# Optimization experiments

Hardware: AMD Instinct MI355X
Metric: run time of the kernel (lower is better)

## Reference

```python
import jax, jax.numpy as jnp
from jax import lax
import numpy as np

FEAT_W = 52      # feature map width/height
IMG_W = 210      # input image width/height
SUB = IMG_W // FEAT_W  # = 4, sub_sample stride
N_ANCHOR = 9
NMS_THRESH = 0.7
PRE_NMS = 12000
POST_NMS = 2000
MIN_SIZE = 16.0


def make_anchors():
    # Faithful vectorization of generateAnchors: outer loop over ctr_x, inner over ctr_y,
    # then c unpacked as (ctr_y, ctr_x) = (x_val, y_val); ratios outer, scales inner.
    vals = (np.arange(SUB, (FEAT_W + 1) * SUB, SUB) - SUB // 2).astype(np.float64)  # 2,6,...,210
    cy = np.repeat(vals, FEAT_W)   # outer loop value -> anchor ctr_y
    cx = np.tile(vals, FEAT_W)     # inner loop value -> anchor ctr_x
    ratios = np.array([0.5, 1.0, 2.0])
    scales = np.array([4.0, 8.0, 16.0])
    h = (SUB * scales[None, :] * np.sqrt(ratios[:, None])).reshape(-1)      # (9,)
    w = (SUB * scales[None, :] * np.sqrt(1.0 / ratios[:, None])).reshape(-1)
    a = np.stack([cy[:, None] - h / 2.0, cx[:, None] - w / 2.0,
                  cy[:, None] + h / 2.0, cx[:, None] + w / 2.0], axis=-1)   # (2704, 9, 4)
    return a.reshape(-1, 4).astype(np.float32)  # (24336, 4) as [y1,x1,y2,x2]

_ANCHORS = jnp.asarray(make_anchors())


def _conv(x, w, b):
    y = lax.conv_general_dilated(x, w, (1, 1), 'SAME',
                                 dimension_numbers=('NCHW', 'OIHW', 'NCHW'))
    return y + b[None, :, None, None]


def propose_regions(locs, obj):
    # locs: (1, 24336, 4); obj: (1, 24336)
    anc = _ANCHORS
    ah = anc[:, 2] - anc[:, 0]
    aw = anc[:, 3] - anc[:, 1]
    acy = anc[:, 0] + 0.5 * ah
    acx = anc[:, 1] + 0.5 * aw
    l = locs[0]
    s = obj[0]
    cy = l[:, 0] * ah + acy
    cx = l[:, 1] * aw + acx
    hh = jnp.exp(l[:, 2]) * ah
    ww = jnp.exp(l[:, 3]) * aw
    roi = jnp.stack([cy - 0.5 * hh, cx - 0.5 * ww,
                     cy + 0.5 * hh, cx + 0.5 * ww], axis=1)
    roi = jnp.clip(roi, 0.0, float(IMG_W))
    hs = roi[:, 2] - roi[:, 0]
    ws = roi[:, 3] - roi[:, 1]
    valid = (hs >= MIN_SIZE) & (ws >= MIN_SIZE)
    # min_size filter folded into score masking; invalid boxes start suppressed
    masked = jnp.where(valid, s, -jnp.inf)
    order = jnp.argsort(-masked)[:PRE_NMS]
    boxes = roi[order]          # (PRE_NMS, 4) sorted by descending score
    v = valid[order]
    sgb = lax.stop_gradient(boxes)
    areas = (sgb[:, 3] - sgb[:, 1] + 1.0) * (sgb[:, 2] - sgb[:, 0] + 1.0)
    idxs = jnp.arange(PRE_NMS)

    def body(supp, i):
        b = sgb[i]
        yy1 = jnp.maximum(b[0], sgb[:, 0])
        xx1 = jnp.maximum(b[1], sgb[:, 1])
        yy2 = jnp.minimum(b[2], sgb[:, 2])
        xx2 = jnp.minimum(b[3], sgb[:, 3])
        inter = jnp.maximum(0.0, xx2 - xx1 + 1.0) * jnp.maximum(0.0, yy2 - yy1 + 1.0)
        iou = inter / (areas[i] + areas - inter)
        new = supp | ((iou > NMS_THRESH) & (idxs > i))
        return jnp.where(supp[i], supp, new), None

    supp, _ = lax.scan(body, ~v, idxs)  # greedy sequential NMS, fixed length
    keep = ~supp
    rank = jnp.cumsum(keep.astype(jnp.int32)) - 1
    write = keep & (rank < POST_NMS)
    tgt = jnp.where(write, rank, POST_NMS)  # overflow/dropped rows go to scrap slot
    out = jnp.zeros((POST_NMS + 1, 4), boxes.dtype).at[tgt].set(
        jnp.where(write[:, None], boxes, 0.0))
    return out[:POST_NMS]  # (2000, 4), zero-padded


def _forward(x, conv1_w, conv1_b, reg_w, reg_b, cls_w, cls_b):
    h = _conv(x, conv1_w, conv1_b)        # (1,256,52,52), no activation (as in source)
    reg = _conv(h, reg_w, reg_b)          # (1,36,52,52)
    cls = _conv(h, cls_w, cls_b)          # (1,18,52,52)
    locs = jnp.transpose(reg, (0, 2, 3, 1)).reshape(1, -1, 4)          # (1,24336,4)
    cls_t = jnp.transpose(cls, (0, 2, 3, 1))                            # (1,52,52,18)
    obj = cls_t.reshape(1, FEAT_W, FEAT_W, N_ANCHOR, 2)[..., 1].reshape(1, -1)
    cls_scores = cls_t.reshape(1, -1, 2)                                # (1,24336,2)
    rois = propose_regions(locs, obj)
    return rois, locs, cls_scores, obj


def setup_inputs() -> dict:
    key = jax.random.key(0)
    ks = jax.random.split(key, 4)
    x = jax.random.normal(ks[0], (1, 256, FEAT_W, FEAT_W), jnp.float32)
    conv1_w = 0.01 * jax.random.normal(ks[1], (256, 256, 3, 3), jnp.float32)
    conv1_b = jnp.zeros((256,), jnp.float32)
    reg_w = 0.01 * jax.random.normal(ks[2], (N_ANCHOR * 4, 256, 1, 1), jnp.float32)
    reg_b = jnp.zeros((N_ANCHOR * 4,), jnp.float32)
    cls_w = 0.01 * jax.random.normal(ks[3], (N_ANCHOR * 2, 256, 1, 1), jnp.float32)
    cls_b = jnp.zeros((N_ANCHOR * 2,), jnp.float32)
    return {"x": x, "conv1_w": conv1_w, "conv1_b": conv1_b,
            "reg_w": reg_w, "reg_b": reg_b, "cls_w": cls_w, "cls_b": cls_b}


def reference(x, conv1_w, conv1_b, reg_w, reg_b, cls_w, cls_b):
    rois, locs, cls_scores, obj = _forward(x, conv1_w, conv1_b, reg_w, reg_b, cls_w, cls_b)
    return (rois, locs, cls_scores, obj, cls_scores)
```

## Files before the change

### kernel.cpp

```cpp
#include <hip/hip_runtime.h>

typedef unsigned long long u64;
typedef unsigned int u32;

#define FEAT 52
#define NPIX 2704
#define NANC 24336
#define PRE  12000
#define POST 2000
#define ROWW 192
#define PADW 54
#define PADS 2916

#define ROIS_OFF 0
#define LOCS_OFF 8000
#define CLS_OFF  105344
#define OBJ_OFF  154016
#define CLS2_OFF 178352

#define OFF_W64   0ull
#define OFF_H64   4718592ull
#define OFF_REG64 10256384ull
#define OFF_SC64  11035136ull
#define OFF_ROI64 11229824ull
#define OFF_KEYS  12008576ull
#define OFF_SBOX  12270720ull
#define OFF_SAREA 12663936ull
#define OFF_SUPP  12762240ull
#define OFF_MASK  12763776ull
#define OFF_XPAD  OFF_MASK

__global__ __launch_bounds__(256) void k_prepx(const float* __restrict__ x,
                                               float* __restrict__ xpad) {
    int t = blockIdx.x * 256 + threadIdx.x;
    int ci = t / PADS, pos = t % PADS;
    int iy = pos / PADW, ix = pos % PADW;
    float v = 0.f;
    if (iy >= 1 && iy <= 52 && ix >= 1 && ix <= 52)
        v = x[ci * NPIX + (iy - 1) * FEAT + (ix - 1)];
    xpad[t] = v;
}

__global__ __launch_bounds__(256) void k_prepw(const float* __restrict__ w,
                                               double* __restrict__ w64) {
    int t = blockIdx.x * 256 + threadIdx.x;
    int j = t & 3;
    int r = t >> 2;
    int k = r % 9;
    int r2 = r / 9;
    int ci = r2 & 255;
    int g = r2 >> 8;
    w64[t] = (double)w[(((g * 4 + j) * 256) + ci) * 9 + k];
}

__global__ __launch_bounds__(256) void k_conv3(const float* __restrict__ xpad,
                                               const double* __restrict__ w64,
                                               const float* __restrict__ b,
                                               double* __restrict__ h64) {
    const int p = blockIdx.x * 256 + threadIdx.x;
    const int o0 = blockIdx.y * 4;
    if (p >= NPIX) return;
    const int y = p / FEAT, xq = p % FEAT;
    double a0 = (double)b[o0+0], a1 = (double)b[o0+1];
    double a2 = (double)b[o0+2], a3 = (double)b[o0+3];
    const float* xb = xpad + y * PADW + xq;
    const double* wb = w64 + (size_t)blockIdx.y * 9216;
    #pragma unroll 2
    for (int ci = 0; ci < 256; ++ci) {
        float f0 = xb[0],   f1 = xb[1],   f2 = xb[2];
        float f3 = xb[54],  f4 = xb[55],  f5 = xb[56];
        float f6 = xb[108], f7 = xb[109], f8 = xb[110];
        double xv[9];
        xv[0]=(double)f0; xv[1]=(double)f1; xv[2]=(double)f2;
        xv[3]=(double)f3; xv[4]=(double)f4; xv[5]=(double)f5;
        xv[6]=(double)f6; xv[7]=(double)f7; xv[8]=(double)f8;
        const double* wr = wb + ci * 36;
        #pragma unroll
        for (int k = 0; k < 9; ++k) {
            a0 += xv[k] * wr[4*k+0];
            a1 += xv[k] * wr[4*k+1];
            a2 += xv[k] * wr[4*k+2];
            a3 += xv[k] * wr[4*k+3];
        }
        xb += PADS;
    }
    h64[(o0+0)*NPIX + p] = a0;
    h64[(o0+1)*NPIX + p] = a1;
    h64[(o0+2)*NPIX + p] = a2;
    h64[(o0+3)*NPIX + p] = a3;
}

__global__ __launch_bounds__(64) void k_conv1(const double* __restrict__ h64,
                                              const float* __restrict__ regw,
                                              const float* __restrict__ regb,
                                              const float* __restrict__ clsw,
                                              const float* __restrict__ clsb,
                                              float* __restrict__ out,
                                              double* __restrict__ reg64,
                                              double* __restrict__ score64) {
    const int g = blockIdx.y;
    const int p = blockIdx.x * 64 + threadIdx.x;
    if (p >= NPIX) return;
    const bool isreg = (g < 4);
    const float* wbase = isreg ? (regw + g * 9 * 256) : (clsw + (g - 4) * 9 * 256);
    const float* bbase = isreg ? (regb + g * 9)       : (clsb + (g - 4) * 9);
    double acc[9];
    #pragma unroll
    for (int j = 0; j < 9; ++j) acc[j] = (double)bbase[j];
    #pragma unroll 4
    for (int ci = 0; ci < 256; ++ci) {
        double h = h64[ci * NPIX + p];
        #pragma unroll
        for (int j = 0; j < 9; ++j)
            acc[j] += h * (double)wbase[j * 256 + ci];
    }
    #pragma unroll
    for (int j = 0; j < 9; ++j) {
        int oc = g * 9 + j;
        float v = (float)acc[j];
        if (isreg) {
            out[LOCS_OFF + p*36 + oc] = v;
            reg64[p*36 + oc] = acc[j];
        } else {
            int c = oc - 36;
            out[CLS_OFF  + p*18 + c] = v;
            out[CLS2_OFF + p*18 + c] = v;
            if (c & 1) {
                out[OBJ_OFF + p*9 + (c >> 1)] = v;
                score64[p*9 + (c >> 1)] = acc[j];
            }
        }
    }
}

__global__ __launch_bounds__(256) void k_decode(const double* __restrict__ reg64,
                                                const double* __restrict__ score64,
                                                double* __restrict__ roi64,
                                                u64* __restrict__ keys) {
    int t = blockIdx.x * 256 + threadIdx.x;
    if (t >= NANC) { keys[t] = ~0ull; return; }
    int pos = t / 9, a = t % 9;
    int py = pos / FEAT, px = pos % FEAT;
    int ri = a / 3, si = a % 3;
    double rat = (ri == 0) ? 0.5 : (ri == 1 ? 1.0 : 2.0);
    double scl = (si == 0) ? 4.0 : (si == 1 ? 8.0 : 16.0);
    double hA = 4.0 * scl * sqrt(rat);
    double wA = 4.0 * scl * sqrt(1.0 / rat);
    double cy0 = 4.0 * py + 2.0, cx0 = 4.0 * px + 2.0;
    float y1f = (float)(cy0 - hA / 2.0), x1f = (float)(cx0 - wA / 2.0);
    float y2f = (float)(cy0 + hA / 2.0), x2f = (float)(cx0 + wA / 2.0);
    double ah = (double)y2f - (double)y1f, aw = (double)x2f - (double)x1f;
    double acy = (double)y1f + 0.5 * ah, acx = (double)x1f + 0.5 * aw;
    double l0 = reg64[4*t+0], l1 = reg64[4*t+1], l2 = reg64[4*t+2], l3 = reg64[4*t+3];
    double cy = l0 * ah + acy, cx = l1 * aw + acx;
    double hh = exp(l2) * ah,  ww = exp(l3) * aw;
    double r0 = fmin(fmax(cy - 0.5*hh, 0.0), 210.0);
    double r1 = fmin(fmax(cx - 0.5*ww, 0.0), 210.0);
    double r2 = fmin(fmax(cy + 0.5*hh, 0.0), 210.0);
    double r3 = fmin(fmax(cx + 0.5*ww, 0.0), 210.0);
    roi64[4*t+0] = r0; roi64[4*t+1] = r1; roi64[4*t+2] = r2; roi64[4*t+3] = r3;
    bool valid = (r2 - r0 >= 16.0) && (r3 - r1 >= 16.0);
    double m = valid ? score64[t] : -__builtin_huge_val();
    long long ll = __double_as_longlong(m);
    u64 u = (u64)ll;
    u64 mono = (ll < 0) ? ~u : (u ^ 0x8000000000000000ull);
    keys[t] = ((~mono) & 0xFFFFFFFFFFFF0000ull) | (u64)t;
}

__global__ __launch_bounds__(1024) void k_sortA(u64* __restrict__ keys) {
    __shared__ u64 s[8192];
    const int base = blockIdx.x * 8192;
    for (int t = threadIdx.x; t < 8192; t += 1024) s[t] = keys[base + t];
    __syncthreads();
    for (int k = 2; k <= 8192; k <<= 1) {
        for (int j = k >> 1; j > 0; j >>= 1) {
            for (int q = threadIdx.x; q < 4096; q += 1024) {
                int i = ((q & ~(j-1)) << 1) | (q & (j-1));
                int l = i | j;
                bool asc = (((base + i) & k) == 0);
                u64 A = s[i], B = s[l];
                bool sw = asc ? (A > B) : (A < B);
                if (sw) { s[i] = B; s[l] = A; }
            }
            __syncthreads();
        }
    }
    for (int t = threadIdx.x; t < 8192; t += 1024) keys[base + t] = s[t];
}

__global__ __launch_bounds__(1024) void k_sortB(u64* __restrict__ keys, int k) {
    __shared__ u64 s[8192];
    const int base = blockIdx.x * 8192;
    for (int t = threadIdx.x; t < 8192; t += 1024) s[t] = keys[base + t];
    __syncthreads();
    for (int j = 4096; j > 0; j >>= 1) {
        for (int q = threadIdx.x; q < 4096; q += 1024) {
            int i = ((q & ~(j-1)) << 1) | (q & (j-1));
            int l = i | j;
            bool asc = (((base + i) & k) == 0);
            u64 A = s[i], B = s[l];
            bool sw = asc ? (A > B) : (A < B);
            if (sw) { s[i] = B; s[l] = A; }
        }
        __syncthreads();
    }
    for (int t = threadIdx.x; t < 8192; t += 1024) keys[base + t] = s[t];
}

__global__ __launch_bounds__(256) void k_sortG(u64* __restrict__ keys, int k, int j) {
    int t = blockIdx.x * 256 + threadIdx.x;
    int i = ((t & ~(j-1)) << 1) | (t & (j-1));
    int l = i | j;
    bool asc = ((i & k) == 0);
    u64 A = keys[i], B = keys[l];
    bool sw = asc ? (A > B) : (A < B);
    if (sw) { keys[i] = B; keys[l] = A; }
}

__global__ __launch_bounds__(256) void k_gather(const u64* __restrict__ keys,
                                                const double* __restrict__ roi64,
                                                double* __restrict__ sbox,
                                                double* __restrict__ sarea,
                                                u64* __restrict__ suppinit) {
    int p = blockIdx.x * 256 + threadIdx.x;
    bool sup = true;
    if (p < PRE) {
        int idx = (int)(keys[p] & 0xFFFFull);
        double b0 = roi64[4*idx+0], b1 = roi64[4*idx+1];
        double b2 = roi64[4*idx+2], b3 = roi64[4*idx+3];
        sbox[4*p+0] = b0; sbox[4*p+1] = b1; sbox[4*p+2] = b2; sbox[4*p+3] = b3;
        sarea[p] = (b3 - b1 + 1.0) * (b2 - b0 + 1.0);
        sup = !((b2 - b0 >= 16.0) && (b3 - b1 >= 16.0));
    } else {
        sbox[4*p+0] = 0.0; sbox[4*p+1] = 0.0; sbox[4*p+2] = 0.0; sbox[4*p+3] = 0.0;
        sarea[p] = 1.0;
    }
    u64 ball = __ballot(sup);
    if ((threadIdx.x & 63) == 0) suppinit[p >> 6] = ball;
}

__global__ __launch_bounds__(256) void k_mask(const double* __restrict__ sbox,
                                              const double* __restrict__ sarea,
                                              u64* __restrict__ mask) {
    const int jt = blockIdx.x, it = blockIdx.y;
    const int ib = it * 64, jb0 = jt * 1024;
    if (jb0 + 1023 <= ib) {
        for (int t = threadIdx.x; t < 1024; t += 256) {
            int ti = t >> 4, w = t & 15;
            int i = ib + ti;
            if (i < PRE) mask[(size_t)i * ROWW + jt*16 + w] = 0ull;
        }
        return;
    }
    __shared__ double jbx[4096];
    __shared__ double jar[1024];
    for (int t = threadIdx.x; t < 4096; t += 256) jbx[t] = sbox[(size_t)jb0*4 + t];
    for (int t = threadIdx.x; t < 1024; t += 256) jar[t] = sarea[jb0 + t];
    __syncthreads();
    int ti = threadIdx.x >> 2;
    int i = ib + ti;
    if (i >= PRE) return;
    double iy1 = sbox[4*i+0], ix1 = sbox[4*i+1], iy2 = sbox[4*i+2], ix2 = sbox[4*i+3];
    double iar = sarea[i];
    for (int w = (threadIdx.x & 3); w < 16; w += 4) {
        u64 bits = 0ull;
        int q0 = w * 64;
        for (int l = 0; l < 64; ++l) {
            int q = q0 + l;
            double jy1 = jbx[4*q+0], jx1 = jbx[4*q+1], jy2 = jbx[4*q+2], jx2 = jbx[4*q+3];
            double yy1 = fmax(iy1, jy1), xx1 = fmax(ix1, jx1);
            double yy2 = fmin(iy2, jy2), xx2 = fmin(ix2, jx2);
            double iw = fmax(xx2 - xx1 + 1.0, 0.0);
            double ih = fmax(yy2 - yy1 + 1.0, 0.0);
            double inter = iw * ih;
            bool s = ((jb0 + q) > i) && (inter > 0.7 * (iar + jar[q] - inter));
            bits |= ((u64)s) << l;
        }
        mask[(size_t)i * ROWW + jt*16 + w] = bits;
    }
}

__device__ inline u64 rdl64(u64 v, int l) {
    u32 lo = (u32)__builtin_amdgcn_readlane((int)(u32)v, l);
    u32 hi = (u32)__builtin_amdgcn_readlane((int)(u32)(v >> 32), l);
    return ((u64)hi << 32) | (u64)lo;
}
#define RFL64(lo, hi) ( ((u64)(u32)__builtin_amdgcn_readfirstlane((int)(hi)) << 32) \
                      | (u64)(u32)__builtin_amdgcn_readfirstlane((int)(lo)) )

__global__ __launch_bounds__(1024) void k_scan(const u64* __restrict__ mask,
                                               const u64* __restrict__ suppinit,
                                               const double* __restrict__ sbox,
                                               float* __restrict__ rois) {
    __shared__ u64 dbuf[2][4608];
    __shared__ u32 keptLDS[POST];
    __shared__ u32 supp8[2][16];
    __shared__ int rankS, doneS;
    const int tid = threadIdx.x;
    const u32* suppinit32 = (const u32*)suppinit;

    if (tid < 16) supp8[0][tid] = suppinit32[tid];
    if (tid == 0) { rankS = 0; doneS = 0; }
    for (int q = tid; q < 4096; q += 1024) {
        int r = q >> 3, w = q & 7;
        dbuf[0][r*9 + w] = (r < PRE) ? mask[(size_t)r * ROWW + w] : 0ull;
    }
    __syncthreads();

    for (int c = 0; c < 24; ++c) {
        const int nc = c + 1;
        const int cb = c & 1, nb = nc & 1;
        if (tid < 64) {
            const int lane = tid;
            if (lane < 16 && nc < 24) supp8[nb][lane] = suppinit32[nc*16 + lane];
            u64 i0 = RFL64(supp8[cb][0],  supp8[cb][1]);
            u64 i1 = RFL64(supp8[cb][2],  supp8[cb][3]);
            u64 i2 = RFL64(supp8[cb][4],  supp8[cb][5]);
            u64 i3 = RFL64(supp8[cb][6],  supp8[cb][7]);
            u64 i4 = RFL64(supp8[cb][8],  supp8[cb][9]);
            u64 i5 = RFL64(supp8[cb][10], supp8[cb][11]);
            u64 i6 = RFL64(supp8[cb][12], supp8[cb][13]);
            u64 i7 = RFL64(supp8[cb][14], supp8[cb][15]);
            u64 a0=0,a1=0,a2=0,a3=0,a4=0,a5=0,a6=0,a7=0;
            int rk = __builtin_amdgcn_readfirstlane(rankS);
            bool dn = false;
#define GROUP(G)                                                                \
            if (!dn) {                                                          \
                u64 z = ~(i##G | a##G);                                         \
                if (z) {                                                        \
                    const u64* rowp = &dbuf[cb][(G*64 + lane)*9];               \
                    u64 r0=rowp[0],r1=rowp[1],r2=rowp[2],r3=rowp[3];            \
                    u64 r4=rowp[4],r5=rowp[5],r6=rowp[6],r7=rowp[7];            \
                    u64 keptm = 0;                                              \
                    while (z) {                                                 \
                        int bpos = (int)__builtin_ctzll(z);                     \
                        u64 q0=rdl64(r0,bpos), q1=rdl64(r1,bpos);               \
                        u64 q2=rdl64(r2,bpos), q3=rdl64(r3,bpos);               \
                        u64 q4=rdl64(r4,bpos), q5=rdl64(r5,bpos);               \
                        u64 q6=rdl64(r6,bpos), q7=rdl64(r7,bpos);               \
                        keptm |= (1ull << bpos);                                \
                        z &= ~(1ull << bpos) & ~q##G;                           \
                        a0|=q0; a1|=q1; a2|=q2; a3|=q3;                         \
                        a4|=q4; a5|=q5; a6|=q6; a7|=q7;                         \
                    }                                                           \
                    int pc = __builtin_popcountll(keptm);                       \
                    int navail = POST - rk;                                     \
                    int mylot = __builtin_amdgcn_mbcnt_hi((u32)(keptm >> 32),   \
                                 __builtin_amdgcn_mbcnt_lo((u32)keptm, 0));     \
                    if (((keptm >> lane) & 1) && mylot < navail)                \
                        keptLDS[rk + mylot] = (u32)(c*512 + G*64 + lane);       \
                    if (pc >= navail) { rk = POST; dn = true; }                 \
                    else rk += pc;                                              \
                }                                                               \
            }
            GROUP(0) GROUP(1) GROUP(2) GROUP(3)
            GROUP(4) GROUP(5) GROUP(6) GROUP(7)
#undef GROUP
            if (lane == 0) { rankS = rk; if (dn) doneS = 1; }
        } else if (nc < 24) {
            for (int q = tid - 64; q < 4096; q += 960) {
                int r = q >> 3, w = q & 7;
                int i = nc*512 + r;
                dbuf[nb][r*9 + w] = (i < PRE) ? mask[(size_t)i * ROWW + nc*8 + w] : 0ull;
            }
        }
        __syncthreads();
        if (doneS || nc >= 24) break;
        {
            int rk = rankS;
            int w = tid & 7;
            u64 acc = 0;
            for (int k = tid >> 3; k < rk; k += 128)
                acc |= mask[(size_t)keptLDS[k] * ROWW + nc*8 + w];
            if (acc) {
                atomicOr(&supp8[nb][2*w],     (u32)acc);
                atomicOr(&supp8[nb][2*w + 1], (u32)(acc >> 32));
            }
        }
        __syncthreads();
    }
    __syncthreads();
    const int R = rankS;
    for (int r = tid; r < POST; r += 1024) {
        if (r < R) {
            int p = (int)keptLDS[r];
            rois[4*r+0] = (float)sbox[4*p+0];
            rois[4*r+1] = (float)sbox[4*p+1];
            rois[4*r+2] = (float)sbox[4*p+2];
            rois[4*r+3] = (float)sbox[4*p+3];
        }
    }
}

extern "C" void kernel_launch(void* const* d_in, const int* in_sizes, int n_in,
                              void* d_out, int out_size, void* d_ws, size_t ws_size,
                              hipStream_t stream) {
    const float* x    = (const float*)d_in[0];
    const float* w1   = (const float*)d_in[1];
    const float* b1   = (const float*)d_in[2];
    const float* regw = (const float*)d_in[3];
    const float* regb = (const float*)d_in[4];
    const float* clsw = (const float*)d_in[5];
    const float* clsb = (const float*)d_in[6];
    float* out = (float*)d_out;

    char* ws = (char*)d_ws;
    double* w64    = (double*)(ws + OFF_W64);
    double* h64    = (double*)(ws + OFF_H64);
    double* reg64  = (double*)(ws + OFF_REG64);
    double* sc64   = (double*)(ws + OFF_SC64);
    double* roi64  = (double*)(ws + OFF_ROI64);
    u64*    keys   = (u64*)   (ws + OFF_KEYS);
    double* sbox   = (double*)(ws + OFF_SBOX);
    double* sarea  = (double*)(ws + OFF_SAREA);
    u64*    supp0  = (u64*)   (ws + OFF_SUPP);
    u64*    maskp  = (u64*)   (ws + OFF_MASK);
    float*  xpad   = (float*) (ws + OFF_XPAD);

    hipMemsetAsync(d_out, 0, 8000 * sizeof(float), stream);

    k_prepx<<<2916, 256, 0, stream>>>(x, xpad);
    k_prepw<<<2304, 256, 0, stream>>>(w1, w64);
    k_conv3<<<dim3(11, 64), 256, 0, stream>>>(xpad, w64, b1, h64);
    k_conv1<<<dim3(43, 6), 64, 0, stream>>>(h64, regw, regb, clsw, clsb, out, reg64, sc64);
    k_decode<<<128, 256, 0, stream>>>(reg64, sc64, roi64, keys);

    k_sortA<<<4, 1024, 0, stream>>>(keys);
    k_sortG<<<64, 256, 0, stream>>>(keys, 16384, 8192);
    k_sortB<<<4, 1024, 0, stream>>>(keys, 16384);
    k_sortG<<<64, 256, 0, stream>>>(keys, 32768, 16384);
    k_sortG<<<64, 256, 0, stream>>>(keys, 32768, 8192);
    k_sortB<<<4, 1024, 0, stream>>>(keys, 32768);

    k_gather<<<48, 256, 0, stream>>>(keys, roi64, sbox, sarea, supp0);
    k_mask<<<dim3(12, 188), 256, 0, stream>>>(sbox, sarea, maskp);
    k_scan<<<1, 1024, 0, stream>>>(maskp, supp0, sbox, out + ROIS_OFF);
}
```

Baseline: 674.3 us.

## Split conv3 over input channels and overlap suppression OR in NMS scan

The 3x3 conv is split into two halves over input channels via a z grid dimension. This doubles the number of blocks for occupancy, and the partial sums are added when conv1 reads them. The sequential NMS scan kernel drops to 512 threads. A dedicated group of waves now ORs the suppression rows of boxes kept in earlier chunks while the scanning wave processes the current chunk, so only newly kept boxes are handled after the barrier. It also loads dbuf rows only on active lanes and prefetches suppinit two chunks ahead. The split conv adds an extra 5.5MB double buffer write and read, and the h64b workspace offset must not overlap other live buffers.

```diff
diff --git a/kernel.cpp b/kernel.cpp
--- a/kernel.cpp
+++ b/kernel.cpp
@@ -29,6 +29,7 @@
 #define OFF_SUPP  12762240ull
 #define OFF_MASK  12763776ull
 #define OFF_XPAD  OFF_MASK
+#define OFF_H64B  (OFF_MASK + 2985984ull)
 
 __global__ __launch_bounds__(256) void k_prepx(const float* __restrict__ x,
                                                float* __restrict__ xpad) {
@@ -56,17 +57,25 @@
 __global__ __launch_bounds__(256) void k_conv3(const float* __restrict__ xpad,
                                                const double* __restrict__ w64,
                                                const float* __restrict__ b,
-                                               double* __restrict__ h64) {
+                                               double* __restrict__ h64,
+                                               double* __restrict__ h64b) {
     const int p = blockIdx.x * 256 + threadIdx.x;
     const int o0 = blockIdx.y * 4;
+    const int half = blockIdx.z;
     if (p >= NPIX) return;
     const int y = p / FEAT, xq = p % FEAT;
-    double a0 = (double)b[o0+0], a1 = (double)b[o0+1];
-    double a2 = (double)b[o0+2], a3 = (double)b[o0+3];
-    const float* xb = xpad + y * PADW + xq;
-    const double* wb = w64 + (size_t)blockIdx.y * 9216;
+    double a0, a1, a2, a3;
+    if (half == 0) {
+        a0 = (double)b[o0+0]; a1 = (double)b[o0+1];
+        a2 = (double)b[o0+2]; a3 = (double)b[o0+3];
+    } else {
+        a0 = a1 = a2 = a3 = 0.0;
+    }
+    const int c0 = half << 7;
+    const float* xb = xpad + (size_t)c0 * PADS + y * PADW + xq;
+    const double* wb = w64 + (size_t)blockIdx.y * 9216 + c0 * 36;
     #pragma unroll 2
-    for (int ci = 0; ci < 256; ++ci) {
+    for (int ci = 0; ci < 128; ++ci) {
         float f0 = xb[0],   f1 = xb[1],   f2 = xb[2];
         float f3 = xb[54],  f4 = xb[55],  f5 = xb[56];
         float f6 = xb[108], f7 = xb[109], f8 = xb[110];
@@ -84,13 +93,15 @@
         }
         xb += PADS;
     }
-    h64[(o0+0)*NPIX + p] = a0;
-    h64[(o0+1)*NPIX + p] = a1;
-    h64[(o0+2)*NPIX + p] = a2;
-    h64[(o0+3)*NPIX + p] = a3;
+    double* ho = (half == 0) ? h64 : h64b;
+    ho[(o0+0)*NPIX + p] = a0;
+    ho[(o0+1)*NPIX + p] = a1;
+    ho[(o0+2)*NPIX + p] = a2;
+    ho[(o0+3)*NPIX + p] = a3;
 }
 
 __global__ __launch_bounds__(64) void k_conv1(const double* __restrict__ h64,
+                                              const double* __restrict__ h64b,
                                               const float* __restrict__ regw,
                                               const float* __restrict__ regb,
                                               const float* __restrict__ clsw,
@@ -109,7 +120,7 @@
     for (int j = 0; j < 9; ++j) acc[j] = (double)bbase[j];
     #pragma unroll 4
     for (int ci = 0; ci < 256; ++ci) {
-        double h = h64[ci * NPIX + p];
+        double h = h64[ci * NPIX + p] + h64b[ci * NPIX + p];
         #pragma unroll
         for (int j = 0; j < 9; ++j)
             acc[j] += h * (double)wbase[j * 256 + ci];
@@ -288,10 +299,10 @@
 #define RFL64(lo, hi) ( ((u64)(u32)__builtin_amdgcn_readfirstlane((int)(hi)) << 32) \
                       | (u64)(u32)__builtin_amdgcn_readfirstlane((int)(lo)) )
 
-__global__ __launch_bounds__(1024) void k_scan(const u64* __restrict__ mask,
-                                               const u64* __restrict__ suppinit,
-                                               const double* __restrict__ sbox,
-                                               float* __restrict__ rois) {
+__global__ __launch_bounds__(512) void k_scan(const u64* __restrict__ mask,
+                                              const u64* __restrict__ suppinit,
+                                              const double* __restrict__ sbox,
+                                              float* __restrict__ rois) {
     __shared__ u64 dbuf[2][4608];
     __shared__ u32 keptLDS[POST];
     __shared__ u32 supp8[2][16];
@@ -299,20 +310,21 @@
     const int tid = threadIdx.x;
     const u32* suppinit32 = (const u32*)suppinit;
 
-    if (tid < 16) supp8[0][tid] = suppinit32[tid];
+    if (tid < 16)                 supp8[0][tid]      = suppinit32[tid];
+    else if (tid < 32)            supp8[1][tid - 16] = suppinit32[tid];
     if (tid == 0) { rankS = 0; doneS = 0; }
-    for (int q = tid; q < 4096; q += 1024) {
+    for (int q = tid; q < 4096; q += 512) {
         int r = q >> 3, w = q & 7;
         dbuf[0][r*9 + w] = (r < PRE) ? mask[(size_t)r * ROWW + w] : 0ull;
     }
     __syncthreads();
 
+    int rank0 = 0;
     for (int c = 0; c < 24; ++c) {
         const int nc = c + 1;
         const int cb = c & 1, nb = nc & 1;
         if (tid < 64) {
             const int lane = tid;
-            if (lane < 16 && nc < 24) supp8[nb][lane] = suppinit32[nc*16 + lane];
             u64 i0 = RFL64(supp8[cb][0],  supp8[cb][1]);
             u64 i1 = RFL64(supp8[cb][2],  supp8[cb][3]);
             u64 i2 = RFL64(supp8[cb][4],  supp8[cb][5]);
@@ -328,9 +340,12 @@
             if (!dn) {                                                          \
                 u64 z = ~(i##G | a##G);                                         \
                 if (z) {                                                        \
-                    const u64* rowp = &dbuf[cb][(G*64 + lane)*9];               \
-                    u64 r0=rowp[0],r1=rowp[1],r2=rowp[2],r3=rowp[3];            \
-                    u64 r4=rowp[4],r5=rowp[5],r6=rowp[6],r7=rowp[7];            \
+                    u64 r0=0,r1=0,r2=0,r3=0,r4=0,r5=0,r6=0,r7=0;                \
+                    if ((z >> lane) & 1ull) {                                   \
+                        const u64* rowp = &dbuf[cb][(G*64 + lane)*9];           \
+                        r0=rowp[0]; r1=rowp[1]; r2=rowp[2]; r3=rowp[3];         \
+                        r4=rowp[4]; r5=rowp[5]; r6=rowp[6]; r7=rowp[7];         \
+                    }                                                           \
                     u64 keptm = 0;                                              \
                     while (z) {                                                 \
                         int bpos = (int)__builtin_ctzll(z);                     \
@@ -357,31 +372,54 @@
             GROUP(4) GROUP(5) GROUP(6) GROUP(7)
 #undef GROUP
             if (lane == 0) { rankS = rk; if (dn) doneS = 1; }
-        } else if (nc < 24) {
-            for (int q = tid - 64; q < 4096; q += 960) {
-                int r = q >> 3, w = q & 7;
-                int i = nc*512 + r;
-                dbuf[nb][r*9 + w] = (i < PRE) ? mask[(size_t)i * ROWW + nc*8 + w] : 0ull;
+        } else if (tid < 256) {
+            if (nc < 24) {
+                for (int q = tid - 64; q < 4096; q += 192) {
+                    int r = q >> 3, w = q & 7;
+                    int i = nc*512 + r;
+                    dbuf[nb][r*9 + w] = (i < PRE) ? mask[(size_t)i * ROWW + nc*8 + w] : 0ull;
+                }
             }
+        } else {
+            if (nc < 24 && rank0 > 0) {
+                u64 acc[8] = {0,0,0,0,0,0,0,0};
+                for (int k = tid - 256; k < rank0; k += 256) {
+                    const u64* rp = mask + (size_t)keptLDS[k] * ROWW + nc*8;
+                    #pragma unroll
+                    for (int w = 0; w < 8; ++w) acc[w] |= rp[w];
+                }
+                #pragma unroll
+                for (int w = 0; w < 8; ++w) {
+                    u64 v = acc[w];
+                    #pragma unroll
+                    for (int s = 1; s < 64; s <<= 1)
+                        v |= (u64)__shfl_xor((unsigned long long)v, s, 64);
+                    if ((tid & 63) == 0) {
+                        if ((u32)v)         atomicOr(&supp8[nb][2*w],   (u32)v);
+                        if ((u32)(v >> 32)) atomicOr(&supp8[nb][2*w+1], (u32)(v >> 32));
+                    }
+                }
+            }
         }
         __syncthreads();
-        if (doneS || nc >= 24) break;
+        if (doneS) break;
+        if (nc >= 24) break;
+        const int rk1 = rankS;
         {
-            int rk = rankS;
             int w = tid & 7;
             u64 acc = 0;
-            for (int k = tid >> 3; k < rk; k += 128)
+            for (int k = rank0 + (tid >> 3); k < rk1; k += 64)
                 acc |= mask[(size_t)keptLDS[k] * ROWW + nc*8 + w];
-            if (acc) {
-                atomicOr(&supp8[nb][2*w],     (u32)acc);
-                atomicOr(&supp8[nb][2*w + 1], (u32)(acc >> 32));
-            }
-        }
+            if ((u32)acc)         atomicOr(&supp8[nb][2*w],   (u32)acc);
+            if ((u32)(acc >> 32)) atomicOr(&supp8[nb][2*w+1], (u32)(acc >> 32));
+            if (tid < 16) supp8[cb][tid] = (c + 2 < 24) ? suppinit32[(c+2)*16 + tid] : 0u;
+        }
+        rank0 = rk1;
         __syncthreads();
     }
     __syncthreads();
     const int R = rankS;
-    for (int r = tid; r < POST; r += 1024) {
+    for (int r = tid; r < POST; r += 512) {
         if (r < R) {
             int p = (int)keptLDS[r];
             rois[4*r+0] = (float)sbox[4*p+0];
@@ -416,13 +454,14 @@
     u64*    supp0  = (u64*)   (ws + OFF_SUPP);
     u64*    maskp  = (u64*)   (ws + OFF_MASK);
     float*  xpad   = (float*) (ws + OFF_XPAD);
+    double* h64b   = (double*)(ws + OFF_H64B);
 
     hipMemsetAsync(d_out, 0, 8000 * sizeof(float), stream);
 
     k_prepx<<<2916, 256, 0, stream>>>(x, xpad);
     k_prepw<<<2304, 256, 0, stream>>>(w1, w64);
-    k_conv3<<<dim3(11, 64), 256, 0, stream>>>(xpad, w64, b1, h64);
-    k_conv1<<<dim3(43, 6), 64, 0, stream>>>(h64, regw, regb, clsw, clsb, out, reg64, sc64);
+    k_conv3<<<dim3(11, 64, 2), 256, 0, stream>>>(xpad, w64, b1, h64, h64b);
+    k_conv1<<<dim3(43, 6), 64, 0, stream>>>(h64, h64b, regw, regb, clsw, clsb, out, reg64, sc64);
     k_decode<<<128, 256, 0, stream>>>(reg64, sc64, roi64, keys);
 
     k_sortA<<<4, 1024, 0, stream>>>(keys);
@@ -434,5 +473,5 @@
 
     k_gather<<<48, 256, 0, stream>>>(keys, roi64, sbox, sarea, supp0);
     k_mask<<<dim3(12, 188), 256, 0, stream>>>(sbox, sarea, maskp);
-    k_scan<<<1, 1024, 0, stream>>>(maskp, supp0, sbox, out + ROIS_OFF);
-}
+    k_scan<<<1, 512, 0, stream>>>(maskp, supp0, sbox, out + ROIS_OFF);
+}
```

Result: faster. 635.1 us (-5.8%).
